# Kernel optimization log

Measured on AMD Instinct MI355X. Metric: run time of the kernel, lower is better.

## Reference

```python
import jax, jax.numpy as jnp
import numpy as np

B, S, R, D = 1, 256, 512, 256   # batch, N_seq, N_res, d_node
C, H = 32, 8                     # head dim, n_heads (H*C == D)
LN_EPS = 1e-5


def setup_inputs() -> dict:
    key = jax.random.key(0)
    ks = jax.random.split(key, 8)
    w = 0.02
    return {
        "M_raw": jax.random.normal(ks[0], (B, S, R, D), jnp.float32),
        "ln_scale": jnp.ones((D,), jnp.float32),
        "ln_bias": jnp.zeros((D,), jnp.float32),
        "Wq": jax.random.normal(ks[1], (H * C, D), jnp.float32) * w,
        "Wk": jax.random.normal(ks[2], (H * C, D), jnp.float32) * w,
        "Wv": jax.random.normal(ks[3], (H * C, D), jnp.float32) * w,
        "Wg": jax.random.normal(ks[4], (H * C, D), jnp.float32) * w,
        "bg": jnp.ones((H * C,), jnp.float32),   # FastFold inits gating bias to 1
        "Wo": jax.random.normal(ks[5], (D, H * C), jnp.float32) * w,
        "bo": jnp.zeros((D,), jnp.float32),
    }


def _layernorm(x, scale, bias):
    mu = jnp.mean(x, axis=-1, keepdims=True)
    var = jnp.mean(jnp.square(x - mu), axis=-1, keepdims=True)
    return (x - mu) * jax.lax.rsqrt(var + LN_EPS) * scale + bias


def reference(M_raw, ln_scale, ln_bias, Wq, Wk, Wv, Wg, bg, Wo, bo):
    # transpose so attention runs over the MSA sequence (column) axis
    M = jnp.swapaxes(M_raw, -2, -3)            # [B, R, S, D]
    M = _layernorm(M, ln_scale, ln_bias)

    def proj(W):                                # [B, R, S, H, C]
        return jnp.einsum('brsd,ed->brse', M, W).reshape(B, R, S, H, C)

    q = proj(Wq) * (C ** -0.5)
    k = proj(Wk)
    v = proj(Wv)

    logits = jnp.einsum('brqhc,brkhc->brhqk', q, k)   # [B, R, H, S, S]
    attn = jax.nn.softmax(logits, axis=-1)
    o = jnp.einsum('brhqk,brkhc->brqhc', attn, v).reshape(B, R, S, H * C)

    gate = jax.nn.sigmoid(jnp.einsum('brsd,ed->brse', M, Wg) + bg)
    out = jnp.einsum('brse,de->brsd', gate * o, Wo) + bo  # [B, R, S, D]

    return M_raw + jnp.swapaxes(out, -2, -3)   # [B, S, R, D]
```

## Files before the change

kernel.cpp:

```cpp
#include <hip/hip_runtime.h>
#include <hip/hip_bf16.h>

#define SS 256
#define RR 512
#define DD 256
#define HH 8

typedef __attribute__((ext_vector_type(8))) short s8;
typedef __attribute__((ext_vector_type(4))) float f4;

__device__ __forceinline__ unsigned short f2bf(float f) {
    union { unsigned int u; float f; } v; v.f = f;
    return (unsigned short)((v.u + 0x7FFFu + ((v.u >> 16) & 1u)) >> 16);
}

__device__ __forceinline__ s8 pack8(f4 a, f4 b) {
    union { s8 v; __hip_bfloat162 h[4]; } u;
    u.h[0] = __float22bfloat162_rn(make_float2(a.x, a.y));
    u.h[1] = __float22bfloat162_rn(make_float2(a.z, a.w));
    u.h[2] = __float22bfloat162_rn(make_float2(b.x, b.y));
    u.h[3] = __float22bfloat162_rn(make_float2(b.z, b.w));
    return u.v;
}

#define MFMA __builtin_amdgcn_mfma_f32_16x16x32_bf16

__global__ __launch_bounds__(256) void prep_kernel(
    const float* __restrict__ Mraw,
    const float* __restrict__ lnsc,
    const float* __restrict__ lnbi,
    const float* __restrict__ Wq, const float* __restrict__ Wk,
    const float* __restrict__ Wv, const float* __restrict__ Wg,
    unsigned short* __restrict__ Mn,
    unsigned short* __restrict__ Wb)
{
    const int b   = blockIdx.x;
    const int tid = threadIdx.x;
    if (b < 2048) {
        const int wave = tid >> 6, lane = tid & 63;
        const int row  = lane >> 2;
        const int l4   = lane & 3;
        const int g    = b * 64 + wave * 16 + row;
        const int r = g >> 8, s = g & 255;
        const float* mrow = Mraw + ((size_t)s * RR + r) * DD;
        float sum = 0.f, ss2 = 0.f;
        #pragma unroll
        for (int o = 0; o < 8; ++o) {
            const int d0 = (o * 4 + l4) * 8;
            f4 a = *(const f4*)(mrow + d0);
            f4 c = *(const f4*)(mrow + d0 + 4);
            sum += a.x + a.y + a.z + a.w + c.x + c.y + c.z + c.w;
            ss2 += a.x*a.x + a.y*a.y + a.z*a.z + a.w*a.w
                 + c.x*c.x + c.y*c.y + c.z*c.z + c.w*c.w;
        }
        sum += __shfl_xor(sum, 1); sum += __shfl_xor(sum, 2);
        ss2 += __shfl_xor(ss2, 1); ss2 += __shfl_xor(ss2, 2);
        const float mu   = sum * (1.f / 256.f);
        const float rstd = rsqrtf(ss2 * (1.f / 256.f) - mu * mu + 1e-5f);
        #pragma unroll
        for (int o = 0; o < 8; ++o) {
            const int d0 = (o * 4 + l4) * 8;
            f4 a  = *(const f4*)(mrow + d0);
            f4 c  = *(const f4*)(mrow + d0 + 4);
            f4 s0v = *(const f4*)(lnsc + d0);
            f4 s1v = *(const f4*)(lnsc + d0 + 4);
            f4 b0v = *(const f4*)(lnbi + d0);
            f4 b1v = *(const f4*)(lnbi + d0 + 4);
            f4 na, nb;
            na.x = (a.x - mu) * rstd * s0v.x + b0v.x;
            na.y = (a.y - mu) * rstd * s0v.y + b0v.y;
            na.z = (a.z - mu) * rstd * s0v.z + b0v.z;
            na.w = (a.w - mu) * rstd * s0v.w + b0v.w;
            nb.x = (c.x - mu) * rstd * s1v.x + b1v.x;
            nb.y = (c.y - mu) * rstd * s1v.y + b1v.y;
            nb.z = (c.z - mu) * rstd * s1v.z + b1v.z;
            nb.w = (c.w - mu) * rstd * s1v.w + b1v.w;
            *(s8*)(Mn + (size_t)g * DD + d0) = pack8(na, nb);
        }
    } else {
        const int wb = b - 2048;
        const int m  = wb >> 5;
        const float* src = (m == 0) ? Wq : (m == 1) ? Wk : (m == 2) ? Wv : Wg;
        const float scale = (m == 0) ? 0.17677669529663687f : 1.0f;
        const int idx = (wb & 31) * 2048 + tid * 8;
        f4 a = *(const f4*)(src + idx);
        f4 c = *(const f4*)(src + idx + 4);
        a = a * scale; c = c * scale;
        *(s8*)(Wb + m * 65536 + idx) = pack8(a, c);
    }
}

__global__ __launch_bounds__(256, 3) void attn_kernel(
    const unsigned short* __restrict__ Mn,
    const unsigned short* __restrict__ Wb,
    const float* __restrict__ bg,
    unsigned short* __restrict__ go)
{
    __shared__ unsigned short lds[20480];
    const int wgid = blockIdx.x;
    const int work = (wgid & 7) * 512 + (wgid >> 3);
    const int r    = work >> 3;
    const int h    = work & 7;
    const int tid  = threadIdx.x;
    const int wave = tid >> 6;
    const int lane = tid & 63;
    const int quad = lane >> 4;
    const int m16  = lane & 15;

    char* KbB  = (char*)lds;
    char* VtbB = (char*)(lds + 8192);
    char* scrB = (char*)(lds + 16384 + wave * 1024);

    const unsigned short* Wqb = Wb;
    const unsigned short* Wkb = Wb + 65536;
    const unsigned short* Wvb = Wb + 131072;
    const unsigned short* Wgb = Wb + 196608;

    const int koff = quad * 8;
    float bgv[2];
    bgv[0] = bg[h * 32 + m16];
    bgv[1] = bg[h * 32 + 16 + m16];

    s8 qfrag[4];
    float garr[4][2][4];

    #pragma unroll
    for (int pi = 0; pi < 2; ++pi) {
        const int s0 = (wave * 4 + pi * 2) * 16;
        const unsigned short* a0p = Mn + ((size_t)r * SS + s0 + m16) * DD + koff;
        const unsigned short* a1p = a0p + 16 * DD;

        f4 aq[2][2], ak[2][2], av[2][2], ag[2][2];
        #pragma unroll
        for (int t = 0; t < 2; ++t)
            #pragma unroll
            for (int c = 0; c < 2; ++c) {
                aq[t][c] = f4{0.f, 0.f, 0.f, 0.f}; ak[t][c] = f4{0.f, 0.f, 0.f, 0.f};
                av[t][c] = f4{0.f, 0.f, 0.f, 0.f}; ag[t][c] = f4{0.f, 0.f, 0.f, 0.f};
            }

        #pragma unroll
        for (int ks = 0; ks < 8; ++ks) {
            const s8 a0 = *(const s8*)(a0p + ks * 32);
            const s8 a1 = *(const s8*)(a1p + ks * 32);
            #pragma unroll
            for (int ct = 0; ct < 2; ++ct) {
                const int wr = (h * 32 + ct * 16 + m16) * DD + ks * 32 + koff;
                const s8 bq = *(const s8*)(Wqb + wr);
                const s8 bk = *(const s8*)(Wkb + wr);
                const s8 bv = *(const s8*)(Wvb + wr);
                const s8 bw = *(const s8*)(Wgb + wr);
                aq[0][ct] = MFMA(a0, bq, aq[0][ct], 0, 0, 0);
                ak[0][ct] = MFMA(a0, bk, ak[0][ct], 0, 0, 0);
                av[0][ct] = MFMA(a0, bv, av[0][ct], 0, 0, 0);
                ag[0][ct] = MFMA(a0, bw, ag[0][ct], 0, 0, 0);
                aq[1][ct] = MFMA(a1, bq, aq[1][ct], 0, 0, 0);
                ak[1][ct] = MFMA(a1, bk, ak[1][ct], 0, 0, 0);
                av[1][ct] = MFMA(a1, bv, av[1][ct], 0, 0, 0);
                ag[1][ct] = MFMA(a1, bw, ag[1][ct], 0, 0, 0);
            }
        }

        #pragma unroll
        for (int tt = 0; tt < 2; ++tt) {
            const int i = pi * 2 + tt;
            const int sbase = s0 + tt * 16;
            #pragma unroll
            for (int ct = 0; ct < 2; ++ct)
                #pragma unroll
                for (int j = 0; j < 4; ++j) {
                    const int q = quad * 4 + j;
                    *(unsigned short*)(scrB +
                        ((q * 64 + (ct * 16 + m16) * 2) ^ (((q >> 1) & 3) << 4)))
                        = f2bf(tt ? aq[1][ct][j] : aq[0][ct][j]);
                }
            qfrag[i] = *(const s8*)(scrB +
                (m16 * 64 + ((quad * 16) ^ (((m16 >> 1) & 3) << 4))));
            #pragma unroll
            for (int ct = 0; ct < 2; ++ct)
                #pragma unroll
                for (int j = 0; j < 4; ++j) {
                    const int s = sbase + quad * 4 + j;
                    const int c = ct * 16 + m16;
                    *(unsigned short*)(KbB +
                        ((s * 64 + c * 2) ^ (((s >> 1) & 3) << 4)))
                        = f2bf(tt ? ak[1][ct][j] : ak[0][ct][j]);
                    *(unsigned short*)(VtbB + ((c * 512 + s * 2) ^ ((m16 & 7) << 4)))
                        = f2bf(tt ? av[1][ct][j] : av[0][ct][j]);
                    const float gv = tt ? ag[1][ct][j] : ag[0][ct][j];
                    garr[i][ct][j] = 1.f / (1.f + __expf(-(gv + bgv[ct])));
                }
        }
    }
    __syncthreads();

    #pragma unroll
    for (int i = 0; i < 4; ++i) {
        const int sbase = (wave * 4 + i) * 16;
        f4 lg[16];
        const int krd = (quad * 16) ^ (((m16 >> 1) & 3) << 4);
        #pragma unroll
        for (int t = 0; t < 16; ++t) {
            const s8 b = *(const s8*)(KbB + ((t * 16 + m16) * 64 + krd));
            f4 z = {0.f, 0.f, 0.f, 0.f};
            lg[t] = MFMA(qfrag[i], b, z, 0, 0, 0);
        }
        float sm4[4] = {0.f, 0.f, 0.f, 0.f};
        #pragma unroll
        for (int t = 0; t < 16; ++t)
            #pragma unroll
            for (int j = 0; j < 4; ++j) {
                const float e = __expf(lg[t][j]);
                lg[t][j] = e; sm4[j] += e;
            }
        #pragma unroll
        for (int j = 0; j < 4; ++j) {
            sm4[j] += __shfl_xor(sm4[j], 1);
            sm4[j] += __shfl_xor(sm4[j], 2);
            sm4[j] += __shfl_xor(sm4[j], 4);
            sm4[j] += __shfl_xor(sm4[j], 8);
        }
        f4 o0 = {0.f, 0.f, 0.f, 0.f}, o1 = {0.f, 0.f, 0.f, 0.f};
        const int ard = m16 * 64 + ((quad * 16) ^ (((m16 >> 1) & 3) << 4));
        #pragma unroll
        for (int ks = 0; ks < 8; ++ks) {
            char* pb = scrB + (ks & 1) * 1024;
            #pragma unroll
            for (int tt2 = 0; tt2 < 2; ++tt2) {
                const int t = ks * 2 + tt2;
                #pragma unroll
                for (int j = 0; j < 4; ++j) {
                    const int q = quad * 4 + j;
                    *(unsigned short*)(pb +
                        ((q * 64 + (tt2 * 16 + m16) * 2) ^ (((q >> 1) & 3) << 4)))
                        = f2bf(lg[t][j]);
                }
            }
            const s8 a  = *(const s8*)(pb + ard);
            const s8 b0 = *(const s8*)(VtbB +
                (((m16)      * 512 + ks * 64 + quad * 16) ^ ((m16 & 7) << 4)));
            const s8 b1 = *(const s8*)(VtbB +
                (((16 + m16) * 512 + ks * 64 + quad * 16) ^ ((m16 & 7) << 4)));
            o0 = MFMA(a, b0, o0, 0, 0, 0);
            o1 = MFMA(a, b1, o1, 0, 0, 0);
        }
        #pragma unroll
        for (int j = 0; j < 4; ++j) {
            const float inv = 1.f / sm4[j];
            const int s = sbase + quad * 4 + j;
            unsigned short* gp = go + ((size_t)r * SS + s) * DD + h * 32 + m16;
            gp[0]  = f2bf(o0[j] * garr[i][0][j] * inv);
            gp[16] = f2bf(o1[j] * garr[i][1][j] * inv);
        }
    }
}

__global__ __launch_bounds__(256) void outproj_kernel(
    const unsigned short* __restrict__ go,
    const float* __restrict__ Wo,
    const float* __restrict__ bo,
    const float* __restrict__ Mraw,
    float* __restrict__ out)
{
    __shared__ unsigned short Bt[32768];
    const int bid  = blockIdx.x;
    const int work = (bid & 7) * 512 + (bid >> 3);
    const int gt   = work >> 1;
    const int nh   = work & 1;
    const int tid  = threadIdx.x;
    const int wave = tid >> 6;
    const int lane = tid & 63;
    const int quad = lane >> 4;
    const int m16  = lane & 15;
    const int g0   = gt * 64 + wave * 16;

    char* BtB = (char*)Bt;
    {
        const int lr = tid >> 1;
        const int hf = tid & 1;
        const float* wrow = Wo + (size_t)(nh * 128 + lr) * DD + hf * 128;
        #pragma unroll
        for (int i = 0; i < 16; ++i) {
            const f4 x0 = *(const f4*)(wrow + i * 8);
            const f4 x1 = *(const f4*)(wrow + i * 8 + 4);
            *(s8*)(BtB + ((lr * 512 + hf * 256 + i * 16) ^ ((lr & 7) << 4)))
                = pack8(x0, x1);
        }
    }
    s8 afr[8];
    #pragma unroll
    for (int ks = 0; ks < 8; ++ks)
        afr[ks] = *(const s8*)(go + (size_t)(g0 + m16) * DD + ks * 32 + quad * 8);
    __syncthreads();

    #pragma unroll 2
    for (int nt = 0; nt < 8; ++nt) {
        f4 acc = {0.f, 0.f, 0.f, 0.f};
        const int lrow = nt * 16 + m16;
        #pragma unroll
        for (int ks = 0; ks < 8; ++ks) {
            const s8 b = *(const s8*)(BtB +
                ((lrow * 512 + ks * 64 + quad * 16) ^ ((m16 & 7) << 4)));
            acc = MFMA(afr[ks], b, acc, 0, 0, 0);
        }
        const int n = nh * 128 + nt * 16 + m16;
        const float bov = bo[n];
        #pragma unroll
        for (int j = 0; j < 4; ++j) {
            const int g  = g0 + quad * 4 + j;
            const int rr = g >> 8;
            const int sA = g & 255;
            const size_t oaddr = ((size_t)sA * RR + rr) * DD + n;
            out[oaddr] = acc[j] + bov + Mraw[oaddr];
        }
    }
}

__global__ void sentinel_ws_kernel(unsigned int* out32) {
    out32[0] = 0x44800000u;
}

extern "C" void kernel_launch(void* const* d_in, const int* in_sizes, int n_in,
                              void* d_out, int out_size, void* d_ws, size_t ws_size,
                              hipStream_t stream) {
    const float* Mraw = (const float*)d_in[0];
    const float* lnsc = (const float*)d_in[1];
    const float* lnbi = (const float*)d_in[2];
    const float* Wq   = (const float*)d_in[3];
    const float* Wk   = (const float*)d_in[4];
    const float* Wv   = (const float*)d_in[5];
    const float* Wg   = (const float*)d_in[6];
    const float* bg   = (const float*)d_in[7];
    const float* Wo   = (const float*)d_in[8];
    const float* bo   = (const float*)d_in[9];
    float* out = (float*)d_out;
    unsigned short* go = (unsigned short*)d_ws;

    const size_t need = (size_t)RR * SS * DD * 2;
    if (ws_size < need) {
        sentinel_ws_kernel<<<1, 1, 0, stream>>>((unsigned int*)d_out);
        return;
    }

    unsigned short* Mn = (unsigned short*)d_out;
    unsigned short* Wb = Mn + 33554432;

    prep_kernel<<<2176, 256, 0, stream>>>(Mraw, lnsc, lnbi, Wq, Wk, Wv, Wg,
                                          Mn, Wb);
    attn_kernel<<<4096, 256, 0, stream>>>(Mn, Wb, bg, go);
    outproj_kernel<<<4096, 256, 0, stream>>>(go, Wo, bo, Mraw, out);
}
```

Baseline: 695.6 us.

## Compute transposed logits to vectorize P and V LDS stores, raise occupancy

The QK^T MFMA now runs with operands swapped, so each lane holds four consecutive key positions for one query. The exp'd probabilities can then be packed and written to LDS as single 8-byte stores instead of four 2-byte scalar stores. The row-sum reduction drops to two cross-quad shuffles plus a per-row shuffle at the end. V^T is likewise written with packed 8-byte stores using a changed swizzle key, and the launch bounds request four blocks per CU instead of three, which may force register spills.

New measurement: 721.1 us. 1.04x slower.

```diff
diff --git a/kernel.cpp b/kernel.cpp
--- a/kernel.cpp
+++ b/kernel.cpp
@@ -21,6 +21,13 @@
     u.h[2] = __float22bfloat162_rn(make_float2(b.x, b.y));
     u.h[3] = __float22bfloat162_rn(make_float2(b.z, b.w));
     return u.v;
+}
+
+__device__ __forceinline__ unsigned long long pack4(f4 a) {
+    union { unsigned long long u; __hip_bfloat162 h[2]; } w;
+    w.h[0] = __float22bfloat162_rn(make_float2(a[0], a[1]));
+    w.h[1] = __float22bfloat162_rn(make_float2(a[2], a[3]));
+    return w.u;
 }
 
 #define MFMA __builtin_amdgcn_mfma_f32_16x16x32_bf16
@@ -90,7 +97,7 @@
     }
 }
 
-__global__ __launch_bounds__(256, 3) void attn_kernel(
+__global__ __launch_bounds__(256, 4) void attn_kernel(
     const unsigned short* __restrict__ Mn,
     const unsigned short* __restrict__ Wb,
     const float* __restrict__ bg,
@@ -177,7 +184,7 @@
             qfrag[i] = *(const s8*)(scrB +
                 (m16 * 64 + ((quad * 16) ^ (((m16 >> 1) & 3) << 4))));
             #pragma unroll
-            for (int ct = 0; ct < 2; ++ct)
+            for (int ct = 0; ct < 2; ++ct) {
                 #pragma unroll
                 for (int j = 0; j < 4; ++j) {
                     const int s = sbase + quad * 4 + j;
@@ -185,11 +192,15 @@
                     *(unsigned short*)(KbB +
                         ((s * 64 + c * 2) ^ (((s >> 1) & 3) << 4)))
                         = f2bf(tt ? ak[1][ct][j] : ak[0][ct][j]);
-                    *(unsigned short*)(VtbB + ((c * 512 + s * 2) ^ ((m16 & 7) << 4)))
-                        = f2bf(tt ? av[1][ct][j] : av[0][ct][j]);
                     const float gv = tt ? ag[1][ct][j] : ag[0][ct][j];
                     garr[i][ct][j] = 1.f / (1.f + __expf(-(gv + bgv[ct])));
                 }
+                const int c = ct * 16 + m16;
+                const f4 vv = tt ? av[1][ct] : av[0][ct];
+                *(unsigned long long*)(VtbB +
+                    ((c * 512 + (sbase + quad * 4) * 2) ^ ((c & 7) << 4)))
+                    = pack4(vv);
+            }
         }
     }
     __syncthreads();
@@ -197,44 +208,35 @@
     #pragma unroll
     for (int i = 0; i < 4; ++i) {
         const int sbase = (wave * 4 + i) * 16;
-        f4 lg[16];
+        f4 lgT[16];
         const int krd = (quad * 16) ^ (((m16 >> 1) & 3) << 4);
         #pragma unroll
         for (int t = 0; t < 16; ++t) {
-            const s8 b = *(const s8*)(KbB + ((t * 16 + m16) * 64 + krd));
+            const s8 kf = *(const s8*)(KbB + ((t * 16 + m16) * 64 + krd));
             f4 z = {0.f, 0.f, 0.f, 0.f};
-            lg[t] = MFMA(qfrag[i], b, z, 0, 0, 0);
-        }
-        float sm4[4] = {0.f, 0.f, 0.f, 0.f};
+            lgT[t] = MFMA(kf, qfrag[i], z, 0, 0, 0);
+        }
+        float sm = 0.f;
         #pragma unroll
         for (int t = 0; t < 16; ++t)
             #pragma unroll
             for (int j = 0; j < 4; ++j) {
-                const float e = __expf(lg[t][j]);
-                lg[t][j] = e; sm4[j] += e;
-            }
-        #pragma unroll
-        for (int j = 0; j < 4; ++j) {
-            sm4[j] += __shfl_xor(sm4[j], 1);
-            sm4[j] += __shfl_xor(sm4[j], 2);
-            sm4[j] += __shfl_xor(sm4[j], 4);
-            sm4[j] += __shfl_xor(sm4[j], 8);
-        }
+                const float e = __expf(lgT[t][j]);
+                lgT[t][j] = e; sm += e;
+            }
+        sm += __shfl_xor(sm, 16);
+        sm += __shfl_xor(sm, 32);
         f4 o0 = {0.f, 0.f, 0.f, 0.f}, o1 = {0.f, 0.f, 0.f, 0.f};
-        const int ard = m16 * 64 + ((quad * 16) ^ (((m16 >> 1) & 3) << 4));
+        const int pkey = ((m16 >> 1) & 1) << 4;
+        const int ard  = m16 * 64 + ((quad * 16) ^ pkey);
         #pragma unroll
         for (int ks = 0; ks < 8; ++ks) {
             char* pb = scrB + (ks & 1) * 1024;
             #pragma unroll
             for (int tt2 = 0; tt2 < 2; ++tt2) {
                 const int t = ks * 2 + tt2;
-                #pragma unroll
-                for (int j = 0; j < 4; ++j) {
-                    const int q = quad * 4 + j;
-                    *(unsigned short*)(pb +
-                        ((q * 64 + (tt2 * 16 + m16) * 2) ^ (((q >> 1) & 3) << 4)))
-                        = f2bf(lg[t][j]);
-                }
+                *(unsigned long long*)(pb +
+                    (m16 * 64 + ((tt2 * 32 + quad * 8) ^ pkey))) = pack4(lgT[t]);
             }
             const s8 a  = *(const s8*)(pb + ard);
             const s8 b0 = *(const s8*)(VtbB +
@@ -244,13 +246,16 @@
             o0 = MFMA(a, b0, o0, 0, 0, 0);
             o1 = MFMA(a, b1, o1, 0, 0, 0);
         }
+        float inv[4];
+        #pragma unroll
+        for (int j = 0; j < 4; ++j)
+            inv[j] = 1.f / __shfl(sm, quad * 4 + j);
         #pragma unroll
         for (int j = 0; j < 4; ++j) {
-            const float inv = 1.f / sm4[j];
             const int s = sbase + quad * 4 + j;
             unsigned short* gp = go + ((size_t)r * SS + s) * DD + h * 32 + m16;
-            gp[0]  = f2bf(o0[j] * garr[i][0][j] * inv);
-            gp[16] = f2bf(o1[j] * garr[i][1][j] * inv);
+            gp[0]  = f2bf(o0[j] * garr[i][0][j] * inv[j]);
+            gp[16] = f2bf(o1[j] * garr[i][1][j] * inv[j]);
         }
     }
 }
```
